# Kernel optimization log

Hardware: AMD Instinct MI355X
Metric: run time of the kernel (lower is better)

## Reference

```python
import jax, jax.numpy as jnp
import numpy as np

B, N, D = 16, 2048, 1024


def _linear_params(key, d, scale):
    kw, kb = jax.random.split(key)
    W = jax.random.uniform(kw, (d, d), jnp.float32, -scale, scale)
    b = jax.random.uniform(kb, (d,), jnp.float32, -scale, scale)
    return W, b


def setup_inputs() -> dict:
    key = jax.random.key(0)
    ks = jax.random.split(key, 9)
    scale = 1.0 / np.sqrt(D)  # torch nn.Linear default init range
    x1 = jax.random.normal(ks[0], (B, N, D), jnp.float32)
    x2 = jax.random.normal(ks[1], (B, N, D), jnp.float32)
    Wq, bq = _linear_params(ks[2], D, scale)
    Wk, bk = _linear_params(ks[3], D, scale)
    Wv, bv = _linear_params(ks[4], D, scale)
    W1, b1 = _linear_params(ks[5], D, scale)
    W2, b2 = _linear_params(ks[6], D, scale)
    W3, b3 = _linear_params(ks[7], D, scale)
    # torch init is zeros(1); use small nonzero so output/grad paths are exercised
    gamma = jax.random.normal(ks[8], (1,), jnp.float32) * 0.1
    return {"x1": x1, "x2": x2, "Wq": Wq, "bq": bq, "Wk": Wk, "bk": bk,
            "Wv": Wv, "bv": bv, "W1": W1, "b1": b1, "W2": W2, "b2": b2,
            "W3": W3, "b3": b3, "gamma": gamma}


def reference(x1, x2, Wq, bq, Wk, bk, Wv, bv, W1, b1, W2, b2, W3, b3, gamma):
    # QKV cross-attention (unscaled softmax, as in the torch source)
    q = jnp.einsum('bnd,ed->bne', x1, Wq) + bq
    k = jnp.einsum('bnd,ed->bne', x2, Wk) + bk
    v = jnp.einsum('bnd,ed->bne', x2, Wv) + bv
    energy = jnp.einsum('bik,bjk->bij', q, k)          # [B, N, N]
    attn = jax.nn.softmax(energy, axis=-1)
    out = jnp.einsum('bij,bjk->bik', attn, v)          # [B, N, D]
    # multiscale sigmoid gate: sigmoid(s1 + s2 + s3)
    s = (jnp.einsum('bnd,ed->bne', out, W1) + b1
         + jnp.einsum('bnd,ed->bne', out, W2) + b2
         + jnp.einsum('bnd,ed->bne', out, W3) + b3)
    out = out * jax.nn.sigmoid(s)
    return gamma * out + x1
```

## Files before the change

### kernel.cpp

```cpp
#include <hip/hip_runtime.h>
#include <hip/hip_bf16.h>
#include <hip/hip_fp16.h>
#include <cstdint>

#define B_ 16
#define N_ 2048
#define D_ 1024

typedef __attribute__((ext_vector_type(4))) float f32x4;
typedef __attribute__((ext_vector_type(8))) short s16x8;

typedef __attribute__((address_space(1))) const void* gas_ptr;
typedef __attribute__((address_space(3))) void* las_ptr;

__device__ __forceinline__ void gload16(const void* g, void* l)
{
    __builtin_amdgcn_global_load_lds((gas_ptr)(uintptr_t)g, (las_ptr)(uintptr_t)l, 16, 0, 0);
}

__device__ __forceinline__ ushort f2bf(float f)
{
    union { __hip_bfloat16 h; ushort u; } c;
    c.h = __float2bfloat16(f);
    return c.u;
}
__device__ __forceinline__ float bf2f(ushort u)
{
    union { __hip_bfloat16 h; ushort u; } c;
    c.u = u;
    return __bfloat162float(c.h);
}

__global__ __launch_bounds__(256)
void cvt_bf16(const float* __restrict__ in, ushort* __restrict__ out, long n)
{
    long i = ((long)blockIdx.x * 256 + threadIdx.x) * 8;
    const long stride = (long)gridDim.x * 256 * 8;
    for (; i < n; i += stride) {
        f32x4 a = *(const f32x4*)(in + i);
        f32x4 b = *(const f32x4*)(in + i + 4);
        s16x8 o;
#pragma unroll
        for (int j = 0; j < 4; ++j) { o[j] = (short)f2bf(a[j]); o[4 + j] = (short)f2bf(b[j]); }
        *(s16x8*)(out + i) = o;
    }
}

__global__ __launch_bounds__(256)
void prep_w(const float* __restrict__ Wq, const float* __restrict__ Wk, const float* __restrict__ Wv,
            const float* __restrict__ W1, const float* __restrict__ W2, const float* __restrict__ W3,
            const float* __restrict__ b1, const float* __restrict__ b2, const float* __restrict__ b3,
            ushort* __restrict__ wq, ushort* __restrict__ wk, ushort* __restrict__ wv,
            ushort* __restrict__ wsum, float* __restrict__ bsum)
{
    const long i = ((long)blockIdx.x * 256 + threadIdx.x) * 4;
    if (i < (long)D_ * D_) {
#pragma unroll
        for (int j = 0; j < 4; ++j) {
            wq[i + j] = f2bf(Wq[i + j]);
            wk[i + j] = f2bf(Wk[i + j]);
            wv[i + j] = f2bf(Wv[i + j]);
            wsum[i + j] = f2bf(W1[i + j] + W2[i + j] + W3[i + j]);
        }
        if (i < D_) {
#pragma unroll
            for (int j = 0; j < 4; ++j) bsum[i + j] = b1[i + j] + b2[i + j] + b3[i + j];
        }
    }
}

template<int EPI>
__global__ __launch_bounds__(512, 2)
void gemm256(const ushort* __restrict__ A, const ushort* __restrict__ Bw,
             void* __restrict__ Out, const float* __restrict__ bias,
             int Nn, int K, int NT,
             long sA, long sB, long sO,
             const ushort* __restrict__ outb, const float* __restrict__ x1r,
             const float* __restrict__ gamma)
{
    __shared__ ushort lds[65536];
    const int tid = threadIdx.x;
    const int l = tid & 63;
    const int w = tid >> 6;
    const int wm = w >> 2, wn = w & 3;
    const int lr = l & 15;
    const int c2x = ((((l >> 4) * 16) ^ ((lr & 8) << 2)) >> 1);

    const int gx = gridDim.x, gy = gridDim.y;
    const int nwg = gx * gy * (int)gridDim.z;
    const int orig = ((int)blockIdx.z * gy + blockIdx.y) * gx + blockIdx.x;
    const int swzb = (orig & 7) * (nwg >> 3) + (orig >> 3);
    const int gxy = gx * gy;
    const int bz = swzb / gxy;
    const int rem = swzb - bz * gxy;
    const int by = rem / gx;
    const int bx = rem - by * gx;
    const int m0 = by * 256, n0 = bx * 256;

    const ushort* Ab = A + (long)bz * sA;
    const ushort* Bb = Bw + (long)bz * sB;

    int srow[2], scol[2];
#pragma unroll
    for (int i = 0; i < 2; ++i) {
        const int L = (i * 512 + tid) * 16;
        const int P = L ^ (((L >> 9) & 1) << 5);
        srow[i] = (P >> 6) & 127;
        scol[i] = ((P >> 13) << 5) | ((P & 63) >> 1);
    }
    const int sdst = w * 512;

    f32x4 acc[8][4];
#pragma unroll
    for (int i = 0; i < 8; ++i)
#pragma unroll
        for (int j = 0; j < 4; ++j) acc[i][j] = f32x4{0.f, 0.f, 0.f, 0.f};
    s16x8 a[4][2], b[2][2][2];

#define STAGEH(pl, t)                                                                     \
    if ((t) < NT) {                                                                       \
        const int rb2 = (t) & 1;                                                          \
        const long kk = (long)(t) << 6;                                                   \
        _Pragma("unroll")                                                                 \
        for (int i = 0; i < 2; ++i) {                                                     \
            if ((pl) < 2)                                                                 \
                gload16(Ab + (long)(m0 + (pl) * 128 + srow[i]) * K + kk + scol[i],        \
                        &lds[rb2 * 16384 + (pl) * 8192 + sdst + i * 4096]);               \
            else                                                                          \
                gload16(Bb + (long)(n0 + ((pl) - 2) * 128 + srow[i]) * K + kk + scol[i],  \
                        &lds[32768 + rb2 * 16384 + ((pl) - 2) * 8192 + sdst + i * 4096]); \
        }                                                                                 \
    }

#define LDA_(qm)                                                                           \
    _Pragma("unroll") for (int mi = 0; mi < 4; ++mi)                                       \
    _Pragma("unroll") for (int ks = 0; ks < 2; ++ks)                                       \
        a[mi][ks] = *(const s16x8*)&lds[rbase_a + ks * 4096 + ((qm) * 64 + mi * 16 + lr) * 32 + c2x];

#define LDB_(qn)                                                                           \
    _Pragma("unroll") for (int ni = 0; ni < 2; ++ni)                                       \
    _Pragma("unroll") for (int ks = 0; ks < 2; ++ks)                                       \
        b[qn][ni][ks] = *(const s16x8*)&lds[rbase_b + ks * 4096 +                          \
            ((wn & 1) * 64 + (qn) * 32 + ni * 16 + lr) * 32 + c2x];

#define MM_(qm, qn)                                                                        \
    __builtin_amdgcn_s_setprio(1);                                                         \
    _Pragma("unroll") for (int mi = 0; mi < 4; ++mi)                                       \
    _Pragma("unroll") for (int ni = 0; ni < 2; ++ni)                                       \
    _Pragma("unroll") for (int ks = 0; ks < 2; ++ks)                                       \
        acc[(qm) * 4 + mi][(qn) * 2 + ni] = __builtin_amdgcn_mfma_f32_16x16x32_bf16(       \
            a[mi][ks], b[qn][ni][ks], acc[(qm) * 4 + mi][(qn) * 2 + ni], 0, 0, 0);         \
    __builtin_amdgcn_s_setprio(0);

#define BARR __builtin_amdgcn_s_barrier()

#define KGROUP(tt) {                                                 \
    const int rb = (tt) & 1;                                         \
    const int rbase_a = rb * 16384 + wm * 8192;                      \
    const int rbase_b = 32768 + rb * 16384 + (wn >> 1) * 8192;       \
    LDB_(0); LDA_(0);                                                \
    STAGEH(0, (tt) + 1); STAGEH(1, (tt) + 1);                        \
    STAGEH(2, (tt) + 1); STAGEH(3, (tt) + 1);                        \
    LDB_(1);                                                         \
    MM_(0, 0);                                                       \
    MM_(0, 1);                                                       \
    LDA_(1);                                                         \
    MM_(1, 0);                                                       \
    MM_(1, 1);                                                       \
    asm volatile("s_waitcnt vmcnt(0)" ::: "memory");                 \
    BARR; }

    STAGEH(0, 0); STAGEH(1, 0); STAGEH(2, 0); STAGEH(3, 0);
    asm volatile("s_waitcnt vmcnt(0)" ::: "memory");
    BARR;

    for (int t = 0; t < NT; ++t) KGROUP(t);

#undef KGROUP
#undef STAGEH
#undef LDA_
#undef LDB_
#undef MM_

    float gam = 0.f;
    if (EPI == 3) gam = *gamma;
#pragma unroll
    for (int am = 0; am < 8; ++am) {
#pragma unroll
        for (int an = 0; an < 4; ++an) {
#pragma unroll
            for (int r = 0; r < 4; ++r) {
                const int m = m0 + wm * 128 + am * 16 + (l >> 4) * 4 + r;
                const int n = n0 + wn * 64 + an * 16 + lr;
                const float v = acc[am][an][r];
                const long o = (long)bz * sO + (long)m * Nn + n;
                if (EPI == 0) {
                    ((ushort*)Out)[o] = f2bf(v + bias[n]);
                } else if (EPI == 1) {
                    union { __half h; ushort u; } c;
                    c.h = __float2half(v);
                    ((ushort*)Out)[o] = c.u;
                } else if (EPI == 2) {
                    ((ushort*)Out)[o] = f2bf(v);
                } else if (EPI == 4) {
                    ((ushort*)Out)[o] = f2bf(v + bias[m]);
                } else {
                    const float s = v + bias[n];
                    const float g = 1.f / (1.f + __expf(-s));
                    const float ov = bf2f(outb[(long)m * Nn + n]);
                    ((float*)Out)[o] = gam * ov * g + x1r[(long)m * Nn + n];
                }
            }
        }
    }
}

__global__ __launch_bounds__(256)
void softmax_inplace(ushort* __restrict__ EA)
{
    const long row = blockIdx.x;
    ushort* p = EA + row * N_;
    const int tid = threadIdx.x;
    const int c0 = tid * 8;
    __shared__ float red[8];

    s16x8 raw = *(const s16x8*)(p + c0);
    float v[8];
    float mx = -3.0e38f;
#pragma unroll
    for (int i = 0; i < 8; ++i) {
        union { ushort u; __half h; } c;
        c.u = (ushort)raw[i];
        v[i] = __half2float(c.h);
        mx = fmaxf(mx, v[i]);
    }
#pragma unroll
    for (int off = 32; off > 0; off >>= 1) mx = fmaxf(mx, __shfl_xor(mx, off));
    if ((tid & 63) == 0) red[tid >> 6] = mx;
    __syncthreads();
    mx = fmaxf(fmaxf(red[0], red[1]), fmaxf(red[2], red[3]));

    float s = 0.f;
#pragma unroll
    for (int i = 0; i < 8; ++i) { v[i] = __expf(v[i] - mx); s += v[i]; }
#pragma unroll
    for (int off = 32; off > 0; off >>= 1) s += __shfl_xor(s, off);
    if ((tid & 63) == 0) red[4 + (tid >> 6)] = s;
    __syncthreads();
    s = (red[4] + red[5]) + (red[6] + red[7]);
    const float inv = 1.f / s;

    s16x8 o;
#pragma unroll
    for (int i = 0; i < 8; ++i) o[i] = (short)f2bf(v[i] * inv);
    *(s16x8*)(p + c0) = o;
}

extern "C" void kernel_launch(void* const* d_in, const int* in_sizes, int n_in,
                              void* d_out, int out_size, void* d_ws, size_t ws_size,
                              hipStream_t stream)
{
    const float* x1 = (const float*)d_in[0];
    const float* x2 = (const float*)d_in[1];
    const float* Wq = (const float*)d_in[2];
    const float* bq = (const float*)d_in[3];
    const float* Wk = (const float*)d_in[4];
    const float* bk = (const float*)d_in[5];
    const float* Wv = (const float*)d_in[6];
    const float* bv = (const float*)d_in[7];
    const float* W1 = (const float*)d_in[8];
    const float* b1 = (const float*)d_in[9];
    const float* W2 = (const float*)d_in[10];
    const float* b2 = (const float*)d_in[11];
    const float* W3 = (const float*)d_in[12];
    const float* b3 = (const float*)d_in[13];
    const float* gamma = (const float*)d_in[14];
    float* out = (float*)d_out;

    char* ws = (char*)d_ws;
    const long SZ_XB = (long)B_ * N_ * D_ * 2;
    ushort* x1b  = (ushort*)(ws);
    ushort* x2b  = (ushort*)(ws + SZ_XB);
    ushort* EA   = (ushort*)(ws);
    ushort* wqb  = (ushort*)(ws + 2 * SZ_XB);
    ushort* wkb  = (ushort*)(ws + 2 * SZ_XB + 1L * 2097152);
    ushort* wvb  = (ushort*)(ws + 2 * SZ_XB + 2L * 2097152);
    ushort* wsb  = (ushort*)(ws + 2 * SZ_XB + 3L * 2097152);
    float*  bsum = (float*) (ws + 2 * SZ_XB + 4L * 2097152);
    char* base2  = ws + 2 * SZ_XB + 4L * 2097152 + 4096;
    ushort* Qb   = (ushort*)(base2);
    ushort* Kb   = (ushort*)(base2 + SZ_XB);
    ushort* Vtb  = (ushort*)(base2 + 2 * SZ_XB);
    ushort* outb = Kb;

    const long NE = (long)B_ * N_ * D_;

    cvt_bf16<<<4096, 256, 0, stream>>>(x1, x1b, NE);
    cvt_bf16<<<4096, 256, 0, stream>>>(x2, x2b, NE);
    prep_w<<<1024, 256, 0, stream>>>(Wq, Wk, Wv, W1, W2, W3, b1, b2, b3,
                                     wqb, wkb, wvb, wsb, bsum);

    gemm256<0><<<dim3(4, 128, 1), 512, 0, stream>>>(x1b, wqb, Qb, bq,
        D_, D_, 16, 0, 0, 0, nullptr, nullptr, nullptr);
    gemm256<0><<<dim3(4, 128, 1), 512, 0, stream>>>(x2b, wkb, Kb, bk,
        D_, D_, 16, 0, 0, 0, nullptr, nullptr, nullptr);

    gemm256<4><<<dim3(8, 4, 16), 512, 0, stream>>>(wvb, x2b, Vtb, bv,
        N_, D_, 16, 0, (long)N_ * D_, (long)D_ * N_,
        nullptr, nullptr, nullptr);

    gemm256<1><<<dim3(8, 8, 16), 512, 0, stream>>>(Qb, Kb, EA, nullptr,
        N_, D_, 16, (long)N_ * D_, (long)N_ * D_, (long)N_ * N_,
        nullptr, nullptr, nullptr);

    softmax_inplace<<<B_ * N_, 256, 0, stream>>>(EA);

    gemm256<2><<<dim3(4, 8, 16), 512, 0, stream>>>(EA, Vtb, outb, nullptr,
        D_, N_, 32, (long)N_ * N_, (long)D_ * N_, (long)N_ * D_,
        nullptr, nullptr, nullptr);

    gemm256<3><<<dim3(4, 128, 1), 512, 0, stream>>>(outb, wsb, out, bsum,
        D_, D_, 16, 0, 0, 0, outb, x1, gamma);
}
```

Measured before the change: 748.9 us.

## Fuse fp32-to-bf16 conversion and softmax normalization into GEMM operand loads

Removes the standalone x1/x2 bf16 conversion kernels: the projection GEMMs now read fp32 inputs directly, convert them in registers and write them to LDS. The softmax is split so that a row-stats kernel only computes the max and inverse sum. The attention-times-V GEMM applies exp and normalization while staging the fp16 energy tile into LDS, which avoids rewriting the N×N matrix. In exchange, the async global-to-LDS loads are replaced by register-path loads with conversion work inside the GEMM main loop, which can reduce overlap and add VALU work (exp per element per tile load).

```diff
diff --git a/kernel.cpp b/kernel.cpp
--- a/kernel.cpp
+++ b/kernel.cpp
@@ -30,20 +30,11 @@
     c.u = u;
     return __bfloat162float(c.h);
 }
-
-__global__ __launch_bounds__(256)
-void cvt_bf16(const float* __restrict__ in, ushort* __restrict__ out, long n)
-{
-    long i = ((long)blockIdx.x * 256 + threadIdx.x) * 8;
-    const long stride = (long)gridDim.x * 256 * 8;
-    for (; i < n; i += stride) {
-        f32x4 a = *(const f32x4*)(in + i);
-        f32x4 b = *(const f32x4*)(in + i + 4);
-        s16x8 o;
-#pragma unroll
-        for (int j = 0; j < 4; ++j) { o[j] = (short)f2bf(a[j]); o[4 + j] = (short)f2bf(b[j]); }
-        *(s16x8*)(out + i) = o;
-    }
+__device__ __forceinline__ float h2f(ushort u)
+{
+    union { ushort u; __half h; } c;
+    c.u = u;
+    return __half2float(c.h);
 }
 
 __global__ __launch_bounds__(256)
@@ -69,14 +60,46 @@
     }
 }
 
-template<int EPI>
+__global__ __launch_bounds__(256)
+void rowstats(const ushort* __restrict__ EA, float2* __restrict__ st)
+{
+    const long row = blockIdx.x;
+    const ushort* p = EA + row * N_;
+    const int tid = threadIdx.x;
+    __shared__ float red[8];
+
+    s16x8 raw = *(const s16x8*)(p + tid * 8);
+    float v[8];
+    float mx = -3.0e38f;
+#pragma unroll
+    for (int i = 0; i < 8; ++i) { v[i] = h2f((ushort)raw[i]); mx = fmaxf(mx, v[i]); }
+#pragma unroll
+    for (int off = 32; off > 0; off >>= 1) mx = fmaxf(mx, __shfl_xor(mx, off));
+    if ((tid & 63) == 0) red[tid >> 6] = mx;
+    __syncthreads();
+    mx = fmaxf(fmaxf(red[0], red[1]), fmaxf(red[2], red[3]));
+
+    float s = 0.f;
+#pragma unroll
+    for (int i = 0; i < 8; ++i) s += __expf(v[i] - mx);
+#pragma unroll
+    for (int off = 32; off > 0; off >>= 1) s += __shfl_xor(s, off);
+    if ((tid & 63) == 0) red[4 + (tid >> 6)] = s;
+    __syncthreads();
+    if (tid == 0) {
+        s = (red[4] + red[5]) + (red[6] + red[7]);
+        st[row] = make_float2(mx, 1.f / s);
+    }
+}
+
+template<int EPI, int AM, int BM>
 __global__ __launch_bounds__(512, 2)
-void gemm256(const ushort* __restrict__ A, const ushort* __restrict__ Bw,
+void gemm256(const void* __restrict__ A, const void* __restrict__ Bw,
              void* __restrict__ Out, const float* __restrict__ bias,
              int Nn, int K, int NT,
              long sA, long sB, long sO,
              const ushort* __restrict__ outb, const float* __restrict__ x1r,
-             const float* __restrict__ gamma)
+             const float* __restrict__ gamma, const float2* __restrict__ stats)
 {
     __shared__ ushort lds[65536];
     const int tid = threadIdx.x;
@@ -97,8 +120,10 @@
     const int bx = rem - by * gx;
     const int m0 = by * 256, n0 = bx * 256;
 
-    const ushort* Ab = A + (long)bz * sA;
-    const ushort* Bb = Bw + (long)bz * sB;
+    const ushort* Ab = (const ushort*)A + (long)bz * sA;
+    const ushort* Bb = (const ushort*)Bw + (long)bz * sB;
+    const float* Afp = (const float*)A + (long)bz * sA;
+    const float* Bfp = (const float*)Bw + (long)bz * sB;
 
     int srow[2], scol[2];
 #pragma unroll
@@ -117,19 +142,57 @@
         for (int j = 0; j < 4; ++j) acc[i][j] = f32x4{0.f, 0.f, 0.f, 0.f};
     s16x8 a[4][2], b[2][2][2];
 
-#define STAGEH(pl, t)                                                                     \
-    if ((t) < NT) {                                                                       \
-        const int rb2 = (t) & 1;                                                          \
-        const long kk = (long)(t) << 6;                                                   \
-        _Pragma("unroll")                                                                 \
-        for (int i = 0; i < 2; ++i) {                                                     \
-            if ((pl) < 2)                                                                 \
-                gload16(Ab + (long)(m0 + (pl) * 128 + srow[i]) * K + kk + scol[i],        \
-                        &lds[rb2 * 16384 + (pl) * 8192 + sdst + i * 4096]);               \
-            else                                                                          \
-                gload16(Bb + (long)(n0 + ((pl) - 2) * 128 + srow[i]) * K + kk + scol[i],  \
-                        &lds[32768 + rb2 * 16384 + ((pl) - 2) * 8192 + sdst + i * 4096]); \
-        }                                                                                 \
+#define STAGEH(pl, t)                                                                      \
+    if ((t) < NT) {                                                                        \
+        const int rb2 = (t) & 1;                                                           \
+        const long kk = (long)(t) << 6;                                                    \
+        const int isA = (pl) < 2;                                                          \
+        const int MODE = isA ? AM : BM;                                                    \
+        const int pl2 = isA ? (pl) : (pl) - 2;                                             \
+        const long rowb = isA ? (long)m0 : (long)n0;                                       \
+        const int dstb = (isA ? 0 : 65536) + rb2 * 32768 + pl2 * 16384;                    \
+        if (MODE == 0) {                                                                   \
+            const ushort* op = isA ? Ab : Bb;                                              \
+            _Pragma("unroll")                                                              \
+            for (int i = 0; i < 2; ++i)                                                    \
+                gload16(op + (rowb + pl2 * 128 + srow[i]) * K + kk + scol[i],              \
+                        (char*)lds + dstb + sdst * 2 + i * 8192);                          \
+        } else if (MODE == 1) {                                                            \
+            const float* fop = isA ? Afp : Bfp;                                            \
+            _Pragma("unroll")                                                              \
+            for (int ps = 0; ps < 2; ++ps) {                                               \
+                const int idx = ps * 512 + tid;                                            \
+                const int ksh = idx >> 9, jj = idx & 511;                                  \
+                const int r = jj >> 2, cq = (jj & 3) * 8;                                  \
+                const float* src = fop + (rowb + pl2 * 128 + r) * K + kk + ksh * 32 + cq;  \
+                f32x4 u0 = *(const f32x4*)src;                                             \
+                f32x4 u1 = *(const f32x4*)(src + 4);                                       \
+                s16x8 pk;                                                                  \
+                _Pragma("unroll")                                                          \
+                for (int e = 0; e < 4; ++e) {                                              \
+                    pk[e] = (short)f2bf(u0[e]); pk[4 + e] = (short)f2bf(u1[e]);            \
+                }                                                                          \
+                const int hb = (r * 64 + cq * 2) ^ ((r & 8) << 2);                         \
+                *(s16x8*)((char*)lds + dstb + ksh * 8192 + hb) = pk;                       \
+            }                                                                              \
+        } else {                                                                           \
+            _Pragma("unroll")                                                              \
+            for (int ps = 0; ps < 2; ++ps) {                                               \
+                const int idx = ps * 512 + tid;                                            \
+                const int ksh = idx >> 9, jj = idx & 511;                                  \
+                const int r = jj >> 2, cq = (jj & 3) * 8;                                  \
+                const long grow = rowb + pl2 * 128 + r;                                    \
+                const ushort* src = Ab + grow * K + kk + ksh * 32 + cq;                    \
+                s16x8 hv = *(const s16x8*)src;                                             \
+                const float2 ms = stats[(long)bz * 2048 + grow];                           \
+                s16x8 pk;                                                                  \
+                _Pragma("unroll")                                                          \
+                for (int e = 0; e < 8; ++e)                                                \
+                    pk[e] = (short)f2bf(__expf(h2f((ushort)hv[e]) - ms.x) * ms.y);         \
+                const int hb = (r * 64 + cq * 2) ^ ((r & 8) << 2);                         \
+                *(s16x8*)((char*)lds + dstb + ksh * 8192 + hb) = pk;                       \
+            }                                                                              \
+        }                                                                                  \
     }
 
 #define LDA_(qm)                                                                           \
@@ -167,11 +230,11 @@
     LDA_(1);                                                         \
     MM_(1, 0);                                                       \
     MM_(1, 1);                                                       \
-    asm volatile("s_waitcnt vmcnt(0)" ::: "memory");                 \
+    asm volatile("s_waitcnt vmcnt(0) lgkmcnt(0)" ::: "memory");      \
     BARR; }
 
     STAGEH(0, 0); STAGEH(1, 0); STAGEH(2, 0); STAGEH(3, 0);
-    asm volatile("s_waitcnt vmcnt(0)" ::: "memory");
+    asm volatile("s_waitcnt vmcnt(0) lgkmcnt(0)" ::: "memory");
     BARR;
 
     for (int t = 0; t < NT; ++t) KGROUP(t);
@@ -215,47 +278,6 @@
     }
 }
 
-__global__ __launch_bounds__(256)
-void softmax_inplace(ushort* __restrict__ EA)
-{
-    const long row = blockIdx.x;
-    ushort* p = EA + row * N_;
-    const int tid = threadIdx.x;
-    const int c0 = tid * 8;
-    __shared__ float red[8];
-
-    s16x8 raw = *(const s16x8*)(p + c0);
-    float v[8];
-    float mx = -3.0e38f;
-#pragma unroll
-    for (int i = 0; i < 8; ++i) {
-        union { ushort u; __half h; } c;
-        c.u = (ushort)raw[i];
-        v[i] = __half2float(c.h);
-        mx = fmaxf(mx, v[i]);
-    }
-#pragma unroll
-    for (int off = 32; off > 0; off >>= 1) mx = fmaxf(mx, __shfl_xor(mx, off));
-    if ((tid & 63) == 0) red[tid >> 6] = mx;
-    __syncthreads();
-    mx = fmaxf(fmaxf(red[0], red[1]), fmaxf(red[2], red[3]));
-
-    float s = 0.f;
-#pragma unroll
-    for (int i = 0; i < 8; ++i) { v[i] = __expf(v[i] - mx); s += v[i]; }
-#pragma unroll
-    for (int off = 32; off > 0; off >>= 1) s += __shfl_xor(s, off);
-    if ((tid & 63) == 0) red[4 + (tid >> 6)] = s;
-    __syncthreads();
-    s = (red[4] + red[5]) + (red[6] + red[7]);
-    const float inv = 1.f / s;
-
-    s16x8 o;
-#pragma unroll
-    for (int i = 0; i < 8; ++i) o[i] = (short)f2bf(v[i] * inv);
-    *(s16x8*)(p + c0) = o;
-}
-
 extern "C" void kernel_launch(void* const* d_in, const int* in_sizes, int n_in,
                               void* d_out, int out_size, void* d_ws, size_t ws_size,
                               hipStream_t stream)
@@ -279,46 +301,41 @@
 
     char* ws = (char*)d_ws;
     const long SZ_XB = (long)B_ * N_ * D_ * 2;
-    ushort* x1b  = (ushort*)(ws);
-    ushort* x2b  = (ushort*)(ws + SZ_XB);
     ushort* EA   = (ushort*)(ws);
     ushort* wqb  = (ushort*)(ws + 2 * SZ_XB);
     ushort* wkb  = (ushort*)(ws + 2 * SZ_XB + 1L * 2097152);
     ushort* wvb  = (ushort*)(ws + 2 * SZ_XB + 2L * 2097152);
     ushort* wsb  = (ushort*)(ws + 2 * SZ_XB + 3L * 2097152);
     float*  bsum = (float*) (ws + 2 * SZ_XB + 4L * 2097152);
-    char* base2  = ws + 2 * SZ_XB + 4L * 2097152 + 4096;
+    float2* stats= (float2*)(ws + 2 * SZ_XB + 4L * 2097152 + 4096);
+    char* base2  = ws + 2 * SZ_XB + 4L * 2097152 + 4096 + 262144;
     ushort* Qb   = (ushort*)(base2);
     ushort* Kb   = (ushort*)(base2 + SZ_XB);
     ushort* Vtb  = (ushort*)(base2 + 2 * SZ_XB);
     ushort* outb = Kb;
 
-    const long NE = (long)B_ * N_ * D_;
-
-    cvt_bf16<<<4096, 256, 0, stream>>>(x1, x1b, NE);
-    cvt_bf16<<<4096, 256, 0, stream>>>(x2, x2b, NE);
     prep_w<<<1024, 256, 0, stream>>>(Wq, Wk, Wv, W1, W2, W3, b1, b2, b3,
                                      wqb, wkb, wvb, wsb, bsum);
 
-    gemm256<0><<<dim3(4, 128, 1), 512, 0, stream>>>(x1b, wqb, Qb, bq,
-        D_, D_, 16, 0, 0, 0, nullptr, nullptr, nullptr);
-    gemm256<0><<<dim3(4, 128, 1), 512, 0, stream>>>(x2b, wkb, Kb, bk,
-        D_, D_, 16, 0, 0, 0, nullptr, nullptr, nullptr);
-
-    gemm256<4><<<dim3(8, 4, 16), 512, 0, stream>>>(wvb, x2b, Vtb, bv,
+    gemm256<0, 1, 0><<<dim3(4, 128, 1), 512, 0, stream>>>(x1, wqb, Qb, bq,
+        D_, D_, 16, 0, 0, 0, nullptr, nullptr, nullptr, nullptr);
+    gemm256<0, 1, 0><<<dim3(4, 128, 1), 512, 0, stream>>>(x2, wkb, Kb, bk,
+        D_, D_, 16, 0, 0, 0, nullptr, nullptr, nullptr, nullptr);
+
+    gemm256<4, 0, 1><<<dim3(8, 4, 16), 512, 0, stream>>>(wvb, x2, Vtb, bv,
         N_, D_, 16, 0, (long)N_ * D_, (long)D_ * N_,
-        nullptr, nullptr, nullptr);
-
-    gemm256<1><<<dim3(8, 8, 16), 512, 0, stream>>>(Qb, Kb, EA, nullptr,
+        nullptr, nullptr, nullptr, nullptr);
+
+    gemm256<1, 0, 0><<<dim3(8, 8, 16), 512, 0, stream>>>(Qb, Kb, EA, nullptr,
         N_, D_, 16, (long)N_ * D_, (long)N_ * D_, (long)N_ * N_,
-        nullptr, nullptr, nullptr);
-
-    softmax_inplace<<<B_ * N_, 256, 0, stream>>>(EA);
-
-    gemm256<2><<<dim3(4, 8, 16), 512, 0, stream>>>(EA, Vtb, outb, nullptr,
+        nullptr, nullptr, nullptr, nullptr);
+
+    rowstats<<<B_ * N_, 256, 0, stream>>>(EA, stats);
+
+    gemm256<2, 2, 0><<<dim3(4, 8, 16), 512, 0, stream>>>(EA, Vtb, outb, nullptr,
         D_, N_, 32, (long)N_ * N_, (long)D_ * N_, (long)N_ * D_,
-        nullptr, nullptr, nullptr);
-
-    gemm256<3><<<dim3(4, 128, 1), 512, 0, stream>>>(outb, wsb, out, bsum,
-        D_, D_, 16, 0, 0, 0, outb, x1, gamma);
-}
+        nullptr, nullptr, nullptr, stats);
+
+    gemm256<3, 0, 0><<<dim3(4, 128, 1), 512, 0, stream>>>(outb, wsb, out, bsum,
+        D_, D_, 16, 0, 0, 0, outb, x1, gamma, nullptr);
+}
```

New measurement: 779.3 us. 4.1% more time.

## Load A operand directly from global memory into registers, stage only B in LDS

Applied to the files above, without the earlier changes.

The GEMM kernel stops staging the A tile through shared memory. Each wave now loads its A fragments straight from global memory into registers every k-step, and only B is double-buffered in LDS, which halves the LDS footprint. The aim is to remove the LDS write and read traffic for A and possibly raise occupancy. The cost is uncoalesced-ish 16-byte global loads with no prefetch ahead of the MFMAs, so each k-step waits on global latency. Waves sharing the same A rows also fetch them redundantly.

```diff
diff --git a/kernel.cpp b/kernel.cpp
--- a/kernel.cpp
+++ b/kernel.cpp
@@ -78,7 +78,7 @@
              const ushort* __restrict__ outb, const float* __restrict__ x1r,
              const float* __restrict__ gamma)
 {
-    __shared__ ushort lds[65536];
+    __shared__ ushort lds[32768];
     const int tid = threadIdx.x;
     const int l = tid & 63;
     const int w = tid >> 6;
@@ -100,6 +100,11 @@
     const ushort* Ab = A + (long)bz * sA;
     const ushort* Bb = Bw + (long)bz * sB;
 
+    const ushort* arow[8];
+#pragma unroll
+    for (int am = 0; am < 8; ++am)
+        arow[am] = Ab + (long)(m0 + wm * 128 + am * 16 + lr) * K + ((l >> 4) * 8);
+
     int srow[2], scol[2];
 #pragma unroll
     for (int i = 0; i < 2; ++i) {
@@ -115,27 +120,22 @@
     for (int i = 0; i < 8; ++i)
 #pragma unroll
         for (int j = 0; j < 4; ++j) acc[i][j] = f32x4{0.f, 0.f, 0.f, 0.f};
-    s16x8 a[4][2], b[2][2][2];
-
-#define STAGEH(pl, t)                                                                     \
+    s16x8 a[8][2], b[2][2][2];
+
+#define STAGEB(pl2, t)                                                                    \
     if ((t) < NT) {                                                                       \
         const int rb2 = (t) & 1;                                                          \
         const long kk = (long)(t) << 6;                                                   \
         _Pragma("unroll")                                                                 \
-        for (int i = 0; i < 2; ++i) {                                                     \
-            if ((pl) < 2)                                                                 \
-                gload16(Ab + (long)(m0 + (pl) * 128 + srow[i]) * K + kk + scol[i],        \
-                        &lds[rb2 * 16384 + (pl) * 8192 + sdst + i * 4096]);               \
-            else                                                                          \
-                gload16(Bb + (long)(n0 + ((pl) - 2) * 128 + srow[i]) * K + kk + scol[i],  \
-                        &lds[32768 + rb2 * 16384 + ((pl) - 2) * 8192 + sdst + i * 4096]); \
-        }                                                                                 \
-    }
-
-#define LDA_(qm)                                                                           \
-    _Pragma("unroll") for (int mi = 0; mi < 4; ++mi)                                       \
+        for (int i = 0; i < 2; ++i)                                                       \
+            gload16(Bb + (long)(n0 + (pl2) * 128 + srow[i]) * K + kk + scol[i],           \
+                    &lds[rb2 * 16384 + (pl2) * 8192 + sdst + i * 4096]);                  \
+    }
+
+#define LDALL(tt)                                                                          \
+    _Pragma("unroll") for (int am = 0; am < 8; ++am)                                       \
     _Pragma("unroll") for (int ks = 0; ks < 2; ++ks)                                       \
-        a[mi][ks] = *(const s16x8*)&lds[rbase_a + ks * 4096 + ((qm) * 64 + mi * 16 + lr) * 32 + c2x];
+        a[am][ks] = *(const s16x8*)(arow[am] + (long)(tt) * 64 + ks * 32);
 
 #define LDB_(qn)                                                                           \
     _Pragma("unroll") for (int ni = 0; ni < 2; ++ni)                                       \
@@ -149,36 +149,34 @@
     _Pragma("unroll") for (int ni = 0; ni < 2; ++ni)                                       \
     _Pragma("unroll") for (int ks = 0; ks < 2; ++ks)                                       \
         acc[(qm) * 4 + mi][(qn) * 2 + ni] = __builtin_amdgcn_mfma_f32_16x16x32_bf16(       \
-            a[mi][ks], b[qn][ni][ks], acc[(qm) * 4 + mi][(qn) * 2 + ni], 0, 0, 0);         \
+            a[(qm) * 4 + mi][ks], b[qn][ni][ks], acc[(qm) * 4 + mi][(qn) * 2 + ni], 0, 0, 0); \
     __builtin_amdgcn_s_setprio(0);
 
 #define BARR __builtin_amdgcn_s_barrier()
 
 #define KGROUP(tt) {                                                 \
     const int rb = (tt) & 1;                                         \
-    const int rbase_a = rb * 16384 + wm * 8192;                      \
-    const int rbase_b = 32768 + rb * 16384 + (wn >> 1) * 8192;       \
-    LDB_(0); LDA_(0);                                                \
-    STAGEH(0, (tt) + 1); STAGEH(1, (tt) + 1);                        \
-    STAGEH(2, (tt) + 1); STAGEH(3, (tt) + 1);                        \
+    const int rbase_b = rb * 16384 + (wn >> 1) * 8192;               \
+    LDALL(tt);                                                       \
+    LDB_(0);                                                         \
+    STAGEB(0, (tt) + 1); STAGEB(1, (tt) + 1);                        \
     LDB_(1);                                                         \
     MM_(0, 0);                                                       \
     MM_(0, 1);                                                       \
-    LDA_(1);                                                         \
     MM_(1, 0);                                                       \
     MM_(1, 1);                                                       \
     asm volatile("s_waitcnt vmcnt(0)" ::: "memory");                 \
     BARR; }
 
-    STAGEH(0, 0); STAGEH(1, 0); STAGEH(2, 0); STAGEH(3, 0);
+    STAGEB(0, 0); STAGEB(1, 0);
     asm volatile("s_waitcnt vmcnt(0)" ::: "memory");
     BARR;
 
     for (int t = 0; t < NT; ++t) KGROUP(t);
 
 #undef KGROUP
-#undef STAGEH
-#undef LDA_
+#undef STAGEB
+#undef LDALL
 #undef LDB_
 #undef MM_
 
```

Result: slower. 1.483 ms (+98.1%).
